# Optimization experiments

Hardware: AMD Instinct MI355X
Metric: run time of the kernel (lower is better)

Reference implementation:

```python
import jax, jax.numpy as jnp
import numpy as np

NORM_EPS = 1e-6
QUANT_EPS = 1e-8


def setup_inputs() -> dict:
    key = jax.random.key(0)
    k1, k2 = jax.random.split(key)
    B, S, D_IN, D_OUT = 2, 4096, 2048, 2048
    x = jax.random.normal(k1, (B, S, D_IN), dtype=jnp.float32)
    # master fp32 weights (kaiming-uniform-ish scale)
    weight = jax.random.uniform(k2, (D_OUT, D_IN), dtype=jnp.float32,
                                minval=-1.0, maxval=1.0) * (1.0 / np.sqrt(D_IN))
    norm_weight = jnp.ones((D_IN,), dtype=jnp.float32)
    return {"x": x, "weight": weight, "norm_weight": norm_weight}


def _rmsnorm(x, gain):
    rms = jnp.sqrt(jnp.mean(x * x, axis=-1, keepdims=True) + NORM_EPS)
    return x / rms * gain


def _ternary_quantize(w):
    gamma = jnp.mean(jnp.abs(w))                       # absmean scale (scalar)
    w_q = jnp.clip(jnp.round(w / (gamma + QUANT_EPS)), -1.0, 1.0)
    return w_q, gamma


def reference(x, weight, norm_weight):
    # 1) RMSNorm input
    xn = _rmsnorm(x, norm_weight)
    # 2) ternary-quantize weights {-1,0,+1} with absmean gamma
    w_q, gamma = _ternary_quantize(weight)
    # 3) matmul with ternary weights, 4) scale by gamma
    # xn: [B,S,Din], w_q: [Dout,Din] -> [B,S,Dout]
    return jnp.einsum('bsd,od->bso', xn, w_q) * gamma
```

## Files before the change

kernel.cpp:

```cpp
#include <hip/hip_runtime.h>
#include <hip/hip_bf16.h>
#include <stdint.h>

typedef unsigned short u16;
typedef signed char i8;

#define D_INNER 2048
#define D_OUTER 2048
#define MROWS   8192
#define W_ELEMS (D_OUTER * D_INNER)
#define NPART   1024

#define BM 128
#define BN 128
#define BK 128

typedef __attribute__((ext_vector_type(4))) float f32x4;
typedef __attribute__((ext_vector_type(4))) int   i32x4;

__global__ __launch_bounds__(256) void prep_kernel(const float* __restrict__ x,
                            const float* __restrict__ g,
                            const float* __restrict__ w,
                            i8* __restrict__ xn, float* __restrict__ srow,
                            float* __restrict__ partials) {
  __shared__ float red[4];
  __shared__ float redm[4];
  int t = threadIdx.x;
  int lane = t & 63, wvi = t >> 6;

  if (blockIdx.x >= MROWS) {
    int p = blockIdx.x - MROWS;
    int base = p * 1024;
    float s = 0.f;
#pragma unroll
    for (int r = 0; r < 4; ++r) {
      f32x4 v = ((const f32x4*)w)[base + r * 256 + t];
      s += fabsf(v[0]) + fabsf(v[1]) + fabsf(v[2]) + fabsf(v[3]);
    }
    for (int off = 32; off; off >>= 1) s += __shfl_down(s, off, 64);
    if (lane == 0) red[wvi] = s;
    __syncthreads();
    if (t == 0) partials[p] = red[0] + red[1] + red[2] + red[3];
    return;
  }

  int row = blockIdx.x;
  const f32x4* xr = (const f32x4*)(x + (size_t)row * D_INNER);
  i8* xo = xn + (size_t)row * D_INNER;

  f32x4 v0 = __builtin_nontemporal_load(&xr[t]);
  f32x4 v1 = __builtin_nontemporal_load(&xr[t + 256]);
  const f32x4* gr = (const f32x4*)g;
  f32x4 g0 = gr[t], g1 = gr[t + 256];

  float s = v0[0]*v0[0] + v0[1]*v0[1] + v0[2]*v0[2] + v0[3]*v0[3]
          + v1[0]*v1[0] + v1[1]*v1[1] + v1[2]*v1[2] + v1[3]*v1[3];
  float m = fmaxf(fmaxf(fmaxf(fabsf(v0[0]*g0[0]), fabsf(v0[1]*g0[1])),
                        fmaxf(fabsf(v0[2]*g0[2]), fabsf(v0[3]*g0[3]))),
                  fmaxf(fmaxf(fabsf(v1[0]*g1[0]), fabsf(v1[1]*g1[1])),
                        fmaxf(fabsf(v1[2]*g1[2]), fabsf(v1[3]*g1[3]))));
  for (int off = 32; off; off >>= 1) {
    s += __shfl_down(s, off, 64);
    m = fmaxf(m, __shfl_down(m, off, 64));
  }
  if (lane == 0) { red[wvi] = s; redm[wvi] = m; }
  __syncthreads();
  float total = red[0] + red[1] + red[2] + red[3];
  float rmax  = fmaxf(fmaxf(redm[0], redm[1]), fmaxf(redm[2], redm[3]));
  float invr = 1.0f / sqrtf(total * (1.0f / (float)D_INNER) + 1e-6f);

  float amax = fmaxf(rmax * invr, 1e-12f);
  float step = amax * (1.0f / 127.0f);
  float qs   = 127.0f / amax;
  if (t == 0) srow[row] = step;

  char4 q0, q1;
  float qv;
  qv = fminf(127.f, fmaxf(-127.f, rintf(v0[0]*invr*g0[0]*qs))); q0.x = (i8)(int)qv;
  qv = fminf(127.f, fmaxf(-127.f, rintf(v0[1]*invr*g0[1]*qs))); q0.y = (i8)(int)qv;
  qv = fminf(127.f, fmaxf(-127.f, rintf(v0[2]*invr*g0[2]*qs))); q0.z = (i8)(int)qv;
  qv = fminf(127.f, fmaxf(-127.f, rintf(v0[3]*invr*g0[3]*qs))); q0.w = (i8)(int)qv;
  qv = fminf(127.f, fmaxf(-127.f, rintf(v1[0]*invr*g1[0]*qs))); q1.x = (i8)(int)qv;
  qv = fminf(127.f, fmaxf(-127.f, rintf(v1[1]*invr*g1[1]*qs))); q1.y = (i8)(int)qv;
  qv = fminf(127.f, fmaxf(-127.f, rintf(v1[2]*invr*g1[2]*qs))); q1.z = (i8)(int)qv;
  qv = fminf(127.f, fmaxf(-127.f, rintf(v1[3]*invr*g1[3]*qs))); q1.w = (i8)(int)qv;
  ((char4*)xo)[t]       = q0;
  ((char4*)xo)[t + 256] = q1;
}

__global__ __launch_bounds__(256) void quant_kernel(const float* __restrict__ w,
                             const float* __restrict__ partials,
                             float* __restrict__ gamma_out, i8* __restrict__ wq) {
  f32x4 pv = ((const f32x4*)partials)[threadIdx.x];
  double d = (double)pv[0] + (double)pv[1] + (double)pv[2] + (double)pv[3];
  for (int off = 32; off; off >>= 1) d += __shfl_down(d, off, 64);
  __shared__ double red[4];
  int lane = threadIdx.x & 63, wvi = threadIdx.x >> 6;
  if (lane == 0) red[wvi] = d;
  __syncthreads();
  double total = red[0] + red[1] + red[2] + red[3];
  float gamma = (float)(total * (1.0 / (double)W_ELEMS));
  float inv = 1.0f / (gamma + 1e-8f);
  if (blockIdx.x == 0 && threadIdx.x == 0) *gamma_out = gamma;

  int tid = blockIdx.x * blockDim.x + threadIdx.x;
  int stride = gridDim.x * blockDim.x;
  for (int i = tid; i < W_ELEMS / 4; i += stride) {
    f32x4 v = ((const f32x4*)w)[i];
    char4 q;
    q.x = (i8)(int)fminf(1.f, fmaxf(-1.f, rintf(v[0] * inv)));
    q.y = (i8)(int)fminf(1.f, fmaxf(-1.f, rintf(v[1] * inv)));
    q.z = (i8)(int)fminf(1.f, fmaxf(-1.f, rintf(v[2] * inv)));
    q.w = (i8)(int)fminf(1.f, fmaxf(-1.f, rintf(v[3] * inv)));
    ((char4*)wq)[i] = q;
  }
}

__global__ __launch_bounds__(256) void gemm_bt(const i8* __restrict__ A,
                                               const i8* __restrict__ Bw,
                                               const float* __restrict__ gamma_p,
                                               const float* __restrict__ srow,
                                               float* __restrict__ C) {
  __shared__ __align__(16) i8 As[BM * BK];
  __shared__ __align__(16) i8 Bs[BN * BK];

  int f   = blockIdx.y * 16 + blockIdx.x;
  int xcd = f & 7;
  int gg  = f >> 3;
  int nb  = (xcd >> 2) * 8 + (gg & 7);
  int mb  = (gg >> 3) * 4 + (xcd & 3);
  int bm0 = mb * BM;
  int bn0 = nb * BN;

  int tid  = threadIdx.x;
  int lane = tid & 63;
  int wv   = tid >> 6;
  int wm   = (wv >> 1) * 64;
  int wn   = (wv & 1) * 64;
  int lm   = lane & 15;
  int kg   = lane >> 4;
  int sw   = lm & 7;

  i32x4 acc[4][4] = {};

  const i8* Ag = A  + (size_t)bm0 * D_INNER;
  const i8* Bg = Bw + (size_t)bn0 * D_INNER;

  for (int kt = 0; kt < D_INNER; kt += BK) {
    __syncthreads();
#pragma unroll
    for (int r = 0; r < 4; ++r) {
      int ci = r * 256 + tid;
      int row = ci >> 3;
      int kc = (((ci & 7) ^ (row & 7)) << 4);
      __builtin_amdgcn_global_load_lds(
          (const __attribute__((address_space(1))) void*)(Ag + (size_t)row * D_INNER + kt + kc),
          (__attribute__((address_space(3))) void*)(As + ci * 16), 16, 0, 0);
    }
#pragma unroll
    for (int r = 0; r < 4; ++r) {
      int ci = r * 256 + tid;
      int row = ci >> 3;
      int kc = (((ci & 7) ^ (row & 7)) << 4);
      __builtin_amdgcn_global_load_lds(
          (const __attribute__((address_space(1))) void*)(Bg + (size_t)row * D_INNER + kt + kc),
          (__attribute__((address_space(3))) void*)(Bs + ci * 16), 16, 0, 0);
    }
    __syncthreads();

#pragma unroll
    for (int s = 0; s < 2; ++s) {
      int gsel = s * 4 + kg;
      i32x4 af[4], bb[4];
#pragma unroll
      for (int i = 0; i < 4; ++i)
        af[i] = *(const i32x4*)(As + (wm + i * 16 + lm) * BK + ((gsel ^ sw) << 4));
#pragma unroll
      for (int j = 0; j < 4; ++j)
        bb[j] = *(const i32x4*)(Bs + (wn + j * 16 + lm) * BK + ((gsel ^ sw) << 4));
#pragma unroll
      for (int i = 0; i < 4; ++i)
#pragma unroll
        for (int j = 0; j < 4; ++j)
          acc[i][j] = __builtin_amdgcn_mfma_i32_16x16x64_i8(af[i], bb[j], acc[i][j], 0, 0, 0);
    }
  }

  float gamma = *gamma_p;
#pragma unroll
  for (int i = 0; i < 4; ++i) {
    int row0 = bm0 + wm + i * 16 + kg * 4;
    f32x4 sv = *(const f32x4*)(srow + row0);
#pragma unroll
    for (int j = 0; j < 4; ++j) {
      int col = bn0 + wn + j * 16 + lm;
      i32x4 v = acc[i][j];
#pragma unroll
      for (int r = 0; r < 4; ++r)
        C[(size_t)(row0 + r) * D_OUTER + col] = (float)v[r] * gamma * sv[r];
    }
  }
}

extern "C" void kernel_launch(void* const* d_in, const int* in_sizes, int n_in,
                              void* d_out, int out_size, void* d_ws, size_t ws_size,
                              hipStream_t stream) {
  const float* x = (const float*)d_in[0];
  const float* w = (const float*)d_in[1];
  const float* g = (const float*)d_in[2];
  float* out = (float*)d_out;

  float* gamma_p  = (float*)d_ws;
  float* partials = (float*)((char*)d_ws + 64);
  float* srow     = (float*)((char*)d_ws + 8192);
  i8* xn = (i8*)((char*)d_ws + 8192 + 32768);
  i8* wq = (i8*)((char*)d_ws + 8192 + 32768 + (size_t)MROWS * D_INNER);

  prep_kernel<<<MROWS + NPART, 256, 0, stream>>>(x, g, w, xn, srow, partials);
  quant_kernel<<<2048, 256, 0, stream>>>(w, partials, gamma_p, wq);
  gemm_bt<<<dim3(D_OUTER / BN, MROWS / BM), 256, 0, stream>>>(xn, wq, gamma_p, srow, out);
}
```

Before: 169.4 us.

## Double-buffer LDS tiles in int8 GEMM to overlap global loads with MFMA

The GEMM now keeps two LDS buffers for the A and B tiles and prefetches the next K-tile with global_load_lds while the current tile is consumed by MFMA. A manual vmcnt wait that lets 8 loads stay outstanding, plus raw barriers, replace the two __syncthreads per iteration. The cost is doubled LDS use (64KB per block), which may lower occupancy. The last iteration wraps around and issues a redundant prefetch of tile 0 that is never used. Correctness relies on the manual waitcnt encoding and on the compiler not reordering the LDS reads across the raw barriers.

```diff
diff --git a/kernel.cpp b/kernel.cpp
--- a/kernel.cpp
+++ b/kernel.cpp
@@ -14,6 +14,8 @@
 #define BM 128
 #define BN 128
 #define BK 128
+
+#define WAIT_VMCNT_8 0x0F78
 
 typedef __attribute__((ext_vector_type(4))) float f32x4;
 typedef __attribute__((ext_vector_type(4))) int   i32x4;
@@ -121,8 +123,8 @@
                                                const float* __restrict__ gamma_p,
                                                const float* __restrict__ srow,
                                                float* __restrict__ C) {
-  __shared__ __align__(16) i8 As[BM * BK];
-  __shared__ __align__(16) i8 Bs[BN * BK];
+  __shared__ __align__(16) i8 As[2][BM * BK];
+  __shared__ __align__(16) i8 Bs[2][BN * BK];
 
   int f   = blockIdx.y * 16 + blockIdx.x;
   int xcd = f & 7;
@@ -146,38 +148,42 @@
   const i8* Ag = A  + (size_t)bm0 * D_INNER;
   const i8* Bg = Bw + (size_t)bn0 * D_INNER;
 
-  for (int kt = 0; kt < D_INNER; kt += BK) {
-    __syncthreads();
-#pragma unroll
-    for (int r = 0; r < 4; ++r) {
-      int ci = r * 256 + tid;
-      int row = ci >> 3;
-      int kc = (((ci & 7) ^ (row & 7)) << 4);
-      __builtin_amdgcn_global_load_lds(
-          (const __attribute__((address_space(1))) void*)(Ag + (size_t)row * D_INNER + kt + kc),
-          (__attribute__((address_space(3))) void*)(As + ci * 16), 16, 0, 0);
-    }
-#pragma unroll
-    for (int r = 0; r < 4; ++r) {
-      int ci = r * 256 + tid;
-      int row = ci >> 3;
-      int kc = (((ci & 7) ^ (row & 7)) << 4);
-      __builtin_amdgcn_global_load_lds(
-          (const __attribute__((address_space(1))) void*)(Bg + (size_t)row * D_INNER + kt + kc),
-          (__attribute__((address_space(3))) void*)(Bs + ci * 16), 16, 0, 0);
-    }
-    __syncthreads();
-
+#define STAGE(GP, LP, KOFF)                                                     \
+  _Pragma("unroll")                                                             \
+  for (int r = 0; r < 4; ++r) {                                                 \
+    int ci = r * 256 + tid;                                                     \
+    int row = ci >> 3;                                                          \
+    int kc = (((ci & 7) ^ (row & 7)) << 4);                                     \
+    __builtin_amdgcn_global_load_lds(                                           \
+        (const __attribute__((address_space(1))) void*)(GP + (size_t)row * D_INNER + (KOFF) + kc), \
+        (__attribute__((address_space(3))) void*)((LP) + ci * 16), 16, 0, 0);   \
+  }
+
+  STAGE(Ag, &As[0][0], 0)
+  STAGE(Bg, &Bs[0][0], 0)
+
+  for (int it = 0; it < D_INNER / BK; ++it) {
+    int cur = it & 1, nxt = cur ^ 1;
+    int koff = ((it + 1) & 15) * BK;
+
+    __builtin_amdgcn_s_barrier();
+    STAGE(Ag, &As[nxt][0], koff)
+    STAGE(Bg, &Bs[nxt][0], koff)
+    __builtin_amdgcn_s_waitcnt(WAIT_VMCNT_8);
+    __builtin_amdgcn_s_barrier();
+
+    const i8* Ab = &As[cur][0];
+    const i8* Bb = &Bs[cur][0];
 #pragma unroll
     for (int s = 0; s < 2; ++s) {
       int gsel = s * 4 + kg;
       i32x4 af[4], bb[4];
 #pragma unroll
       for (int i = 0; i < 4; ++i)
-        af[i] = *(const i32x4*)(As + (wm + i * 16 + lm) * BK + ((gsel ^ sw) << 4));
+        af[i] = *(const i32x4*)(Ab + (wm + i * 16 + lm) * BK + ((gsel ^ sw) << 4));
 #pragma unroll
       for (int j = 0; j < 4; ++j)
-        bb[j] = *(const i32x4*)(Bs + (wn + j * 16 + lm) * BK + ((gsel ^ sw) << 4));
+        bb[j] = *(const i32x4*)(Bb + (wn + j * 16 + lm) * BK + ((gsel ^ sw) << 4));
 #pragma unroll
       for (int i = 0; i < 4; ++i)
 #pragma unroll
@@ -185,6 +191,7 @@
           acc[i][j] = __builtin_amdgcn_mfma_i32_16x16x64_i8(af[i], bb[j], acc[i][j], 0, 0, 0);
     }
   }
+#undef STAGE
 
   float gamma = *gamma_p;
 #pragma unroll
```

Result: no change. 170.0 us (+0.4%).
